# Performance work log

Hardware: AMD Instinct MI355X
Metric: run time of the kernel (lower is better)

## Reference

```python
import jax, jax.numpy as jnp
import numpy as np

N, F_IN, H, MH = 50000, 128, 128, 256
E = 800000

def _lin_init(key, out_d, in_d, bias=True):
    k1, k2 = jax.random.split(key)
    bound = 1.0 / np.sqrt(in_d)
    W = jax.random.uniform(k1, (out_d, in_d), minval=-bound, maxval=bound, dtype=jnp.float32)
    if bias:
        b = jax.random.uniform(k2, (out_d,), minval=-bound, maxval=bound, dtype=jnp.float32)
        return W, b
    return W, None

def setup_inputs() -> dict:
    key = jax.random.key(0)
    ks = jax.random.split(key, 8)
    x = jax.random.normal(ks[0], (N, F_IN), dtype=jnp.float32)
    edge_index = jax.random.randint(ks[1], (2, E), 0, N, dtype=jnp.int64)
    W1l, b1l = _lin_init(ks[2], H, F_IN, bias=True)   # SAGEConv1 neighbor lin (with bias)
    W1r, _ = _lin_init(ks[3], H, F_IN, bias=False)    # SAGEConv1 root lin (no bias)
    W2l, b2l = _lin_init(ks[4], H, H, bias=True)
    W2r, _ = _lin_init(ks[5], H, H, bias=False)
    Wm1, bm1 = _lin_init(ks[6], MH, 2 * H, bias=True)
    Wm2, bm2 = _lin_init(ks[7], 1, MH, bias=True)
    return {"x": x, "edge_index": edge_index,
            "W1l": W1l, "b1l": b1l, "W1r": W1r,
            "W2l": W2l, "b2l": b2l, "W2r": W2r,
            "Wm1": Wm1, "bm1": bm1, "Wm2": Wm2, "bm2": bm2}

def _sage_conv(x, src, dst, Wl, bl, Wr, num_nodes):
    # mean-aggregate messages x[src] at dst, then lin_l(agg) + lin_r(x)
    agg = jax.ops.segment_sum(x[src], dst, num_segments=num_nodes)
    cnt = jax.ops.segment_sum(jnp.ones((src.shape[0],), x.dtype), dst, num_segments=num_nodes)
    agg = agg / jnp.maximum(cnt, 1.0)[:, None]
    return agg @ Wl.T + bl + x @ Wr.T

def reference(x, edge_index, W1l, b1l, W1r, W2l, b2l, W2r, Wm1, bm1, Wm2, bm2):
    src, dst = edge_index[0], edge_index[1]
    n = x.shape[0]
    h = jax.nn.relu(_sage_conv(x, src, dst, W1l, b1l, W1r, n))
    # dropout is identity in eval mode
    h = jax.nn.relu(_sage_conv(h, src, dst, W2l, b2l, W2r, n))
    ef = jnp.concatenate([h[src], h[dst]], axis=-1)  # [E, 2H]
    out = jax.nn.relu(ef @ Wm1.T + bm1) @ Wm2.T + bm2
    return out.reshape(-1)
```

## Files before the change

kernel.cpp:

```cpp
#include <hip/hip_runtime.h>
#include <hip/hip_bf16.h>

#define NN 50000
#define F 128
#define EE 800000
#define MHD 256
#define CAP 44

typedef __attribute__((ext_vector_type(8))) short bf16x8;
typedef __attribute__((ext_vector_type(4))) float f32x4;

__device__ __forceinline__ float b2f(unsigned short u) {
    union { unsigned int i; float f; } v; v.i = ((unsigned)u) << 16; return v.f;
}
__device__ __forceinline__ unsigned short f2b(float f) {
    unsigned int x = __float_as_uint(f);
    unsigned int r = x + 0x7fffu + ((x >> 16) & 1u);
    return (unsigned short)(r >> 16);
}

__global__ __launch_bounds__(256) void cast_zero_kernel(
    const float* __restrict__ x,
    const float* __restrict__ W1l, const float* __restrict__ W1r,
    const float* __restrict__ W2l, const float* __restrict__ W2r,
    const float* __restrict__ Wm1, const float* __restrict__ Wm2,
    unsigned short* __restrict__ xb, unsigned short* __restrict__ wb,
    int* __restrict__ cntp, float* __restrict__ w2p) {
    int bid = blockIdx.x;
    if (bid < 6250) {
        int i = (bid * 256 + threadIdx.x) * 4;
        float4 v = *(const float4*)(x + i);
        ushort4 o; o.x = f2b(v.x); o.y = f2b(v.y); o.z = f2b(v.z); o.w = f2b(v.w);
        *(ushort4*)(xb + i) = o;
    } else if (bid < 6378) {
        int i = ((bid - 6250) * 256 + threadIdx.x) * 4;
        unsigned short o[4];
        if (i < 32768) {
            const float* p = (i < 16384) ? (W1l + i) : (W1r + (i - 16384));
            float4 v = *(const float4*)p;
            o[0] = f2b(v.x); o[1] = f2b(v.y); o[2] = f2b(v.z); o[3] = f2b(v.w);
        } else if (i < 65536) {
            int local = i - 32768;
            const float* M = (local < 16384) ? W2l : W2r;
            int lm = local & 16383;
            int n = lm >> 7, kp = lm & 127;
#pragma unroll
            for (int t = 0; t < 4; t++) {
                int k = ((kp + t) & 7) * 16 + ((kp + t) >> 3);
                o[t] = f2b(M[n * 128 + k]);
            }
        } else {
            int local = i - 65536;
            int n = local >> 8, k2 = local & 255;
            int half = k2 >> 7, kp = k2 & 127;
#pragma unroll
            for (int t = 0; t < 4; t++) {
                int k = half * 128 + ((kp + t) & 7) * 16 + ((kp + t) >> 3);
                o[t] = f2b(Wm1[n * 256 + k]);
            }
        }
        *(ushort4*)(wb + i) = *(ushort4*)o;
    } else if (bid < 7160) {
        int idx = ((bid - 6378) * 256 + threadIdx.x) * 4;
        if (idx < NN * 16) *(int4*)(cntp + idx) = (int4){0, 0, 0, 0};
    } else {
        int t = threadIdx.x;
        w2p[t] = Wm2[(t & 15) * 16 + (t >> 4)];
    }
}

__global__ __launch_bounds__(256) void cvt_fill_kernel(
    const int* __restrict__ ei, int* __restrict__ cntp,
    unsigned short* __restrict__ slots) {
    __shared__ int isI64;
    if (threadIdx.x == 0) {
        int z = 0;
        for (int i = 1; i < 128; i += 2) z |= ei[i];
        isI64 = (z == 0) ? 1 : 0;
    }
    __syncthreads();
    int e = blockIdx.x * 256 + threadIdx.x;
    if (e >= EE) return;
    int s, d;
    if (isI64) {
        const long long* e64 = (const long long*)ei;
        s = (int)e64[e];
        d = (int)e64[EE + e];
    } else {
        s = ei[e];
        d = ei[EE + e];
    }
    int pos = atomicAdd(&cntp[d << 4], 1);
    if (pos < CAP) {
        unsigned short* sp = slots + (size_t)d * (CAP * 3) + pos * 3;
        sp[0] = (unsigned short)s;
        sp[1] = (unsigned short)(e & 0xffff);
        sp[2] = (unsigned short)((unsigned)e >> 16);
    }
}

__global__ __launch_bounds__(256) void sage_layer_kernel(
    const unsigned short* __restrict__ xin,
    const unsigned short* __restrict__ slots, const int* __restrict__ cntp,
    int* __restrict__ cnt2,
    const unsigned short* __restrict__ W1, const unsigned short* __restrict__ W2,
    const float* __restrict__ bias,
    unsigned short* __restrict__ out) {
    __shared__ unsigned short lds[4][16][136];
    int wave = threadIdx.x >> 6, lane = threadIdx.x & 63;
    int m0 = (blockIdx.x * 4 + wave) * 16;

    int g = lane >> 4, l16 = lane & 15, col8 = l16 * 8;
    for (int batch = 0; batch < 4; batch++) {
        int node = m0 + batch * 4 + g;
        int n = 0, ctrue = 0;
        const unsigned short* sp = slots;
        if (node < NN) {
            ctrue = cntp[node << 4];
            n = (ctrue < CAP) ? ctrue : CAP;
            sp = slots + (size_t)node * (CAP * 3);
            if (l16 == 0) cnt2[node] = ctrue;
        }
        float a[8] = {0,0,0,0,0,0,0,0};
        float b[8] = {0,0,0,0,0,0,0,0};
        int j = 0;
        for (; j + 7 < n; j += 8) {
            int s0 = sp[(j + 0) * 3], s1 = sp[(j + 1) * 3];
            int s2 = sp[(j + 2) * 3], s3 = sp[(j + 3) * 3];
            int s4 = sp[(j + 4) * 3], s5 = sp[(j + 5) * 3];
            int s6 = sp[(j + 6) * 3], s7 = sp[(j + 7) * 3];
            bf16x8 v0 = *(const bf16x8*)(xin + (size_t)s0 * F + col8);
            bf16x8 v1 = *(const bf16x8*)(xin + (size_t)s1 * F + col8);
            bf16x8 v2 = *(const bf16x8*)(xin + (size_t)s2 * F + col8);
            bf16x8 v3 = *(const bf16x8*)(xin + (size_t)s3 * F + col8);
            bf16x8 v4 = *(const bf16x8*)(xin + (size_t)s4 * F + col8);
            bf16x8 v5 = *(const bf16x8*)(xin + (size_t)s5 * F + col8);
            bf16x8 v6 = *(const bf16x8*)(xin + (size_t)s6 * F + col8);
            bf16x8 v7 = *(const bf16x8*)(xin + (size_t)s7 * F + col8);
            for (int i = 0; i < 8; i++)
                a[i] += (b2f((unsigned short)v0[i]) + b2f((unsigned short)v1[i]))
                      + (b2f((unsigned short)v2[i]) + b2f((unsigned short)v3[i]));
            for (int i = 0; i < 8; i++)
                b[i] += (b2f((unsigned short)v4[i]) + b2f((unsigned short)v5[i]))
                      + (b2f((unsigned short)v6[i]) + b2f((unsigned short)v7[i]));
        }
        for (; j + 3 < n; j += 4) {
            int s0 = sp[(j + 0) * 3], s1 = sp[(j + 1) * 3];
            int s2 = sp[(j + 2) * 3], s3 = sp[(j + 3) * 3];
            bf16x8 v0 = *(const bf16x8*)(xin + (size_t)s0 * F + col8);
            bf16x8 v1 = *(const bf16x8*)(xin + (size_t)s1 * F + col8);
            bf16x8 v2 = *(const bf16x8*)(xin + (size_t)s2 * F + col8);
            bf16x8 v3 = *(const bf16x8*)(xin + (size_t)s3 * F + col8);
            for (int i = 0; i < 8; i++)
                a[i] += (b2f((unsigned short)v0[i]) + b2f((unsigned short)v1[i]))
                      + (b2f((unsigned short)v2[i]) + b2f((unsigned short)v3[i]));
        }
        for (; j < n; j++) {
            int s0 = sp[j * 3];
            bf16x8 v0 = *(const bf16x8*)(xin + (size_t)s0 * F + col8);
            for (int i = 0; i < 8; i++) a[i] += b2f((unsigned short)v0[i]);
        }
        float inv = 1.0f / fmaxf((float)ctrue, 1.0f);
        unsigned short o[8];
        for (int i = 0; i < 8; i++) o[i] = f2b((a[i] + b[i]) * inv);
        *(bf16x8*)&lds[wave][batch * 4 + g][col8] = *(bf16x8*)o;
    }
    __syncthreads();

    int c = lane & 15, q = lane >> 4;
    f32x4 acc[8];
    for (int nt = 0; nt < 8; nt++) {
        float b = bias[nt * 16 + c];
        acc[nt] = (f32x4){b, b, b, b};
    }
    int mrow = m0 + c; if (mrow > NN - 1) mrow = NN - 1;
    for (int op = 0; op < 2; op++) {
        const unsigned short* W = op ? W2 : W1;
        for (int kb = 0; kb < 4; kb++) {
            bf16x8 a;
            if (op == 0) a = *(const bf16x8*)&lds[wave][c][kb * 32 + q * 8];
            else         a = *(const bf16x8*)(xin + (size_t)mrow * F + kb * 32 + q * 8);
            for (int nt = 0; nt < 8; nt++) {
                bf16x8 b = *(const bf16x8*)(W + (size_t)(nt * 16 + c) * F + kb * 32 + q * 8);
                acc[nt] = __builtin_amdgcn_mfma_f32_16x16x32_bf16(a, b, acc[nt], 0, 0, 0);
            }
        }
    }
#pragma unroll
    for (int r = 0; r < 4; r++) {
        int node = m0 + q * 4 + r;
        if (node < NN) {
            unsigned short o[8];
#pragma unroll
            for (int nt = 0; nt < 8; nt++) o[nt] = f2b(fmaxf(acc[nt][r], 0.0f));
            *(bf16x8*)(out + (size_t)node * F + c * 8) = *(bf16x8*)o;
        }
    }
}

__global__ __launch_bounds__(256) void pq_gemm_kernel(
    const unsigned short* __restrict__ h,
    const unsigned short* __restrict__ wmb,
    const float* __restrict__ bm1,
    unsigned short* __restrict__ PQ) {
    int wave = threadIdx.x >> 6, lane = threadIdx.x & 63;
    int c = lane & 15, q = lane >> 4;
    int half = wave >> 1, ntBase = (wave & 1) * 8;
    int m0 = blockIdx.x * 64;
    int mr0 = m0 + c;      if (mr0 > NN - 1) mr0 = NN - 1;
    int mr1 = m0 + 16 + c; if (mr1 > NN - 1) mr1 = NN - 1;
    int mr2 = m0 + 32 + c; if (mr2 > NN - 1) mr2 = NN - 1;
    int mr3 = m0 + 48 + c; if (mr3 > NN - 1) mr3 = NN - 1;
    f32x4 acc0[8], acc1[8], acc2[8], acc3[8];
#pragma unroll
    for (int nt = 0; nt < 8; nt++) {
        float b = half ? bm1[(ntBase + nt) * 16 + c] : 0.0f;
        acc0[nt] = (f32x4){b, b, b, b};
        acc1[nt] = (f32x4){b, b, b, b};
        acc2[nt] = (f32x4){b, b, b, b};
        acc3[nt] = (f32x4){b, b, b, b};
    }
#pragma unroll
    for (int kb = 0; kb < 4; kb++) {
        bf16x8 a0 = *(const bf16x8*)(h + (size_t)mr0 * F + kb * 32 + q * 8);
        bf16x8 a1 = *(const bf16x8*)(h + (size_t)mr1 * F + kb * 32 + q * 8);
        bf16x8 a2 = *(const bf16x8*)(h + (size_t)mr2 * F + kb * 32 + q * 8);
        bf16x8 a3 = *(const bf16x8*)(h + (size_t)mr3 * F + kb * 32 + q * 8);
#pragma unroll
        for (int nt = 0; nt < 8; nt++) {
            bf16x8 b = *(const bf16x8*)(wmb + (size_t)((ntBase + nt) * 16 + c) * 256 + half * 128 + kb * 32 + q * 8);
            acc0[nt] = __builtin_amdgcn_mfma_f32_16x16x32_bf16(a0, b, acc0[nt], 0, 0, 0);
            acc1[nt] = __builtin_amdgcn_mfma_f32_16x16x32_bf16(a1, b, acc1[nt], 0, 0, 0);
            acc2[nt] = __builtin_amdgcn_mfma_f32_16x16x32_bf16(a2, b, acc2[nt], 0, 0, 0);
            acc3[nt] = __builtin_amdgcn_mfma_f32_16x16x32_bf16(a3, b, acc3[nt], 0, 0, 0);
        }
    }
#pragma unroll
    for (int r = 0; r < 4; r++) {
        int n0 = m0 + q * 4 + r;
        int n1 = m0 + 16 + q * 4 + r;
        int n2 = m0 + 32 + q * 4 + r;
        int n3 = m0 + 48 + q * 4 + r;
        unsigned short o[8];
        if (n0 < NN) {
#pragma unroll
            for (int nt = 0; nt < 8; nt++) o[nt] = f2b(acc0[nt][r]);
            *(bf16x8*)(PQ + (size_t)n0 * 512 + half * 256 + c * 16 + ntBase) = *(bf16x8*)o;
        }
        if (n1 < NN) {
#pragma unroll
            for (int nt = 0; nt < 8; nt++) o[nt] = f2b(acc1[nt][r]);
            *(bf16x8*)(PQ + (size_t)n1 * 512 + half * 256 + c * 16 + ntBase) = *(bf16x8*)o;
        }
        if (n2 < NN) {
#pragma unroll
            for (int nt = 0; nt < 8; nt++) o[nt] = f2b(acc2[nt][r]);
            *(bf16x8*)(PQ + (size_t)n2 * 512 + half * 256 + c * 16 + ntBase) = *(bf16x8*)o;
        }
        if (n3 < NN) {
#pragma unroll
            for (int nt = 0; nt < 8; nt++) o[nt] = f2b(acc3[nt][r]);
            *(bf16x8*)(PQ + (size_t)n3 * 512 + half * 256 + c * 16 + ntBase) = *(bf16x8*)o;
        }
    }
}

__global__ __launch_bounds__(256) void edge_dot_kernel(
    const unsigned short* __restrict__ PQ,
    const unsigned short* __restrict__ slots, const int* __restrict__ cnt2,
    const float* __restrict__ w2p, const float* __restrict__ bm2,
    float* __restrict__ out) {
    int wave = threadIdx.x >> 6, lane = threadIdx.x & 63;
    int node = blockIdx.x * 4 + wave;
    if (node >= NN) return;
    int g = lane >> 4, l16 = lane & 15;
    int col = l16 * 16;
    float w2f[16], qf[16];
    *(float4*)(w2f + 0)  = *(const float4*)(w2p + col + 0);
    *(float4*)(w2f + 4)  = *(const float4*)(w2p + col + 4);
    *(float4*)(w2f + 8)  = *(const float4*)(w2p + col + 8);
    *(float4*)(w2f + 12) = *(const float4*)(w2p + col + 12);
    {
        bf16x8 q0 = *(const bf16x8*)(PQ + (size_t)node * 512 + 256 + col);
        bf16x8 q1 = *(const bf16x8*)(PQ + (size_t)node * 512 + 256 + col + 8);
#pragma unroll
        for (int i = 0; i < 8; i++) { qf[i] = b2f((unsigned short)q0[i]); qf[8 + i] = b2f((unsigned short)q1[i]); }
    }
    float b2 = bm2[0];
    int ctrue = cnt2[node];
    int n = (ctrue < CAP) ? ctrue : CAP;
    const unsigned short* sp = slots + (size_t)node * (CAP * 3);
    int j = g;
    for (; j + 4 < n; j += 8) {
        int s0 = sp[j * 3],       s1 = sp[(j + 4) * 3];
        int eid0 = sp[j * 3 + 1] | ((int)sp[j * 3 + 2] << 16);
        int eid1 = sp[(j + 4) * 3 + 1] | ((int)sp[(j + 4) * 3 + 2] << 16);
        uint4 a0 = *(const uint4*)(PQ + (size_t)s0 * 512 + col);
        uint4 a1 = *(const uint4*)(PQ + (size_t)s0 * 512 + col + 8);
        uint4 c0 = *(const uint4*)(PQ + (size_t)s1 * 512 + col);
        uint4 c1 = *(const uint4*)(PQ + (size_t)s1 * 512 + col + 8);
        float t0 = 0.f, t1 = 0.f;
        unsigned int w0[8] = {a0.x, a0.y, a0.z, a0.w, a1.x, a1.y, a1.z, a1.w};
        unsigned int w1[8] = {c0.x, c0.y, c0.z, c0.w, c1.x, c1.y, c1.z, c1.w};
#pragma unroll
        for (int i = 0; i < 8; i++) {
            float lo0 = __uint_as_float(w0[i] << 16);
            float hi0 = __uint_as_float(w0[i] & 0xffff0000u);
            float lo1 = __uint_as_float(w1[i] << 16);
            float hi1 = __uint_as_float(w1[i] & 0xffff0000u);
            t0 += fmaxf(lo0 + qf[2 * i], 0.f) * w2f[2 * i]
                + fmaxf(hi0 + qf[2 * i + 1], 0.f) * w2f[2 * i + 1];
            t1 += fmaxf(lo1 + qf[2 * i], 0.f) * w2f[2 * i]
                + fmaxf(hi1 + qf[2 * i + 1], 0.f) * w2f[2 * i + 1];
        }
        t0 += __shfl_xor(t0, 1);  t1 += __shfl_xor(t1, 1);
        t0 += __shfl_xor(t0, 2);  t1 += __shfl_xor(t1, 2);
        t0 += __shfl_xor(t0, 4);  t1 += __shfl_xor(t1, 4);
        t0 += __shfl_xor(t0, 8);  t1 += __shfl_xor(t1, 8);
        if (l16 == 0) { out[eid0] = t0 + b2; out[eid1] = t1 + b2; }
    }
    for (; j < n; j += 4) {
        int s0 = sp[j * 3];
        int eid0 = sp[j * 3 + 1] | ((int)sp[j * 3 + 2] << 16);
        uint4 a0 = *(const uint4*)(PQ + (size_t)s0 * 512 + col);
        uint4 a1 = *(const uint4*)(PQ + (size_t)s0 * 512 + col + 8);
        unsigned int w0[8] = {a0.x, a0.y, a0.z, a0.w, a1.x, a1.y, a1.z, a1.w};
        float t = 0.f;
#pragma unroll
        for (int i = 0; i < 8; i++) {
            float lo = __uint_as_float(w0[i] << 16);
            float hi = __uint_as_float(w0[i] & 0xffff0000u);
            t += fmaxf(lo + qf[2 * i], 0.f) * w2f[2 * i]
               + fmaxf(hi + qf[2 * i + 1], 0.f) * w2f[2 * i + 1];
        }
        t += __shfl_xor(t, 1);
        t += __shfl_xor(t, 2);
        t += __shfl_xor(t, 4);
        t += __shfl_xor(t, 8);
        if (l16 == 0) out[eid0] = t + b2;
    }
}

extern "C" void kernel_launch(void* const* d_in, const int* in_sizes, int n_in,
                              void* d_out, int out_size, void* d_ws, size_t ws_size,
                              hipStream_t stream) {
    const float* x   = (const float*)d_in[0];
    const int*   ei  = (const int*)d_in[1];
    const float* W1l = (const float*)d_in[2];
    const float* b1l = (const float*)d_in[3];
    const float* W1r = (const float*)d_in[4];
    const float* W2l = (const float*)d_in[5];
    const float* b2l = (const float*)d_in[6];
    const float* W2r = (const float*)d_in[7];
    const float* Wm1 = (const float*)d_in[8];
    const float* bm1 = (const float*)d_in[9];
    const float* Wm2 = (const float*)d_in[10];
    const float* bm2 = (const float*)d_in[11];

    char* ws = (char*)d_ws;
    unsigned short* PQ    = (unsigned short*)(ws);
    unsigned short* xb    = (unsigned short*)(ws);
    unsigned short* h1    = (unsigned short*)(ws + 12800000);
    int*            cntp  = (int*)(ws + 25600000);
    unsigned short* wb    = (unsigned short*)(ws + 51200000);
    float*          w2p   = (float*)(ws + 51462144);
    int*            cnt2  = (int*)(ws + 51463168);
    unsigned short* slots = (unsigned short*)(ws + 51663168);
    unsigned short* h2    = (unsigned short*)(ws + 64863168);
    float*          outp  = (float*)d_out;

    const unsigned short* w1l_b  = wb;
    const unsigned short* w1r_b  = wb + 16384;
    const unsigned short* w2l_p  = wb + 32768;
    const unsigned short* w2r_p  = wb + 49152;
    const unsigned short* wm1_p  = wb + 65536;

    cast_zero_kernel<<<7161, 256, 0, stream>>>(x, W1l, W1r, W2l, W2r, Wm1, Wm2, xb, wb, cntp, w2p);
    cvt_fill_kernel<<<3125, 256, 0, stream>>>(ei, cntp, slots);

    sage_layer_kernel<<<782, 256, 0, stream>>>(xb, slots, cntp, cnt2, w1l_b, w1r_b, b1l, h1);
    sage_layer_kernel<<<782, 256, 0, stream>>>(h1, slots, cntp, cnt2, w2l_p, w2r_p, b2l, h2);
    pq_gemm_kernel<<<782, 256, 0, stream>>>(h2, wm1_p, bm1, PQ);
    edge_dot_kernel<<<12500, 256, 0, stream>>>(PQ, slots, cnt2, w2p, bm2, outp);
}
```

Baseline: 369.8 us.

## Build CSR slots via two-pass bucketing with LDS staging instead of global atomics

Replaces the per-edge global atomic scatter into padded per-node counters and slots with two passes. First edges are binned into coarse buckets of 64 destination nodes, split 8 ways. Then one block per bucket assembles the slot lists in LDS and writes them out contiguously. This avoids scattered global atomics and the write of a 3.2MB zeroed counter array, at the cost of an extra kernel and an intermediate bucket buffer with capacity limits (BCAP=256 per cell) that could silently drop edges under skewed degree.

Measured after the change: 372.4 us. About the same (+0.7%).

```diff
diff --git a/kernel.cpp b/kernel.cpp
--- a/kernel.cpp
+++ b/kernel.cpp
@@ -6,6 +6,8 @@
 #define EE 800000
 #define MHD 256
 #define CAP 44
+#define NBKT 782
+#define BCAP 256
 
 typedef __attribute__((ext_vector_type(8))) short bf16x8;
 typedef __attribute__((ext_vector_type(4))) float f32x4;
@@ -25,7 +27,7 @@
     const float* __restrict__ W2l, const float* __restrict__ W2r,
     const float* __restrict__ Wm1, const float* __restrict__ Wm2,
     unsigned short* __restrict__ xb, unsigned short* __restrict__ wb,
-    int* __restrict__ cntp, float* __restrict__ w2p) {
+    int* __restrict__ bcnt, float* __restrict__ w2p) {
     int bid = blockIdx.x;
     if (bid < 6250) {
         int i = (bid * 256 + threadIdx.x) * 4;
@@ -60,18 +62,18 @@
             }
         }
         *(ushort4*)(wb + i) = *(ushort4*)o;
-    } else if (bid < 7160) {
+    } else if (bid < 6385) {
         int idx = ((bid - 6378) * 256 + threadIdx.x) * 4;
-        if (idx < NN * 16) *(int4*)(cntp + idx) = (int4){0, 0, 0, 0};
+        if (idx < 8 * NBKT) *(int4*)(bcnt + idx) = (int4){0, 0, 0, 0};
     } else {
         int t = threadIdx.x;
         w2p[t] = Wm2[(t & 15) * 16 + (t >> 4)];
     }
 }
 
-__global__ __launch_bounds__(256) void cvt_fill_kernel(
-    const int* __restrict__ ei, int* __restrict__ cntp,
-    unsigned short* __restrict__ slots) {
+__global__ __launch_bounds__(256) void bucket_kernel(
+    const int* __restrict__ ei, int* __restrict__ bcnt,
+    int2* __restrict__ bkt) {
     __shared__ int isI64;
     if (threadIdx.x == 0) {
         int z = 0;
@@ -90,19 +92,54 @@
         s = ei[e];
         d = ei[EE + e];
     }
-    int pos = atomicAdd(&cntp[d << 4], 1);
-    if (pos < CAP) {
-        unsigned short* sp = slots + (size_t)d * (CAP * 3) + pos * 3;
-        sp[0] = (unsigned short)s;
-        sp[1] = (unsigned short)(e & 0xffff);
-        sp[2] = (unsigned short)((unsigned)e >> 16);
+    int cell = (blockIdx.x & 7) * NBKT + (d >> 6);
+    int pos = atomicAdd(&bcnt[cell], 1);
+    if (pos < BCAP) {
+        bkt[(size_t)cell * BCAP + pos] = make_int2((int)((unsigned)s | ((unsigned)d << 16)), e);
+    }
+}
+
+__global__ __launch_bounds__(256) void build_kernel(
+    const int* __restrict__ bcnt, const int2* __restrict__ bkt,
+    unsigned short* __restrict__ slots, int* __restrict__ cnt2) {
+    __shared__ unsigned short stg[64][132];
+    __shared__ int lcnt[64];
+    int b = blockIdx.x, t = threadIdx.x;
+    if (t < 64) lcnt[t] = 0;
+    __syncthreads();
+#pragma unroll
+    for (int seg = 0; seg < 8; seg++) {
+        int cell = seg * NBKT + b;
+        int bc = bcnt[cell]; if (bc > BCAP) bc = BCAP;
+        for (int i = t; i < bc; i += 256) {
+            int2 en = bkt[(size_t)cell * BCAP + i];
+            unsigned v = (unsigned)en.x;
+            int s = (int)(v & 0xffffu);
+            int dl = (int)((v >> 16) & 63u);
+            int pos = atomicAdd(&lcnt[dl], 1);
+            if (pos < CAP) {
+                stg[dl][pos * 3 + 0] = (unsigned short)s;
+                stg[dl][pos * 3 + 1] = (unsigned short)(en.y & 0xffff);
+                stg[dl][pos * 3 + 2] = (unsigned short)((unsigned)en.y >> 16);
+            }
+        }
+    }
+    __syncthreads();
+    for (int v = t; v < 64 * 33; v += 256) {
+        int row = v / 33, off = (v % 33) * 4;
+        int node = b * 64 + row;
+        if (node < NN)
+            *(ushort4*)(slots + (size_t)node * 132 + off) = *(ushort4*)&stg[row][off];
+    }
+    if (t < 64) {
+        int node = b * 64 + t;
+        if (node < NN) cnt2[node] = lcnt[t];
     }
 }
 
 __global__ __launch_bounds__(256) void sage_layer_kernel(
     const unsigned short* __restrict__ xin,
-    const unsigned short* __restrict__ slots, const int* __restrict__ cntp,
-    int* __restrict__ cnt2,
+    const unsigned short* __restrict__ slots, const int* __restrict__ cnt2,
     const unsigned short* __restrict__ W1, const unsigned short* __restrict__ W2,
     const float* __restrict__ bias,
     unsigned short* __restrict__ out) {
@@ -116,10 +153,9 @@
         int n = 0, ctrue = 0;
         const unsigned short* sp = slots;
         if (node < NN) {
-            ctrue = cntp[node << 4];
+            ctrue = cnt2[node];
             n = (ctrue < CAP) ? ctrue : CAP;
             sp = slots + (size_t)node * (CAP * 3);
-            if (l16 == 0) cnt2[node] = ctrue;
         }
         float a[8] = {0,0,0,0,0,0,0,0};
         float b[8] = {0,0,0,0,0,0,0,0};
@@ -361,12 +397,13 @@
     unsigned short* PQ    = (unsigned short*)(ws);
     unsigned short* xb    = (unsigned short*)(ws);
     unsigned short* h1    = (unsigned short*)(ws + 12800000);
-    int*            cntp  = (int*)(ws + 25600000);
+    int2*           bkt   = (int2*)(ws + 25600000);
     unsigned short* wb    = (unsigned short*)(ws + 51200000);
     float*          w2p   = (float*)(ws + 51462144);
     int*            cnt2  = (int*)(ws + 51463168);
-    unsigned short* slots = (unsigned short*)(ws + 51663168);
-    unsigned short* h2    = (unsigned short*)(ws + 64863168);
+    int*            bcnt  = (int*)(ws + 51663168);
+    unsigned short* slots = (unsigned short*)(ws + 51688256);
+    unsigned short* h2    = (unsigned short*)(ws + 64888256);
     float*          outp  = (float*)d_out;
 
     const unsigned short* w1l_b  = wb;
@@ -375,11 +412,12 @@
     const unsigned short* w2r_p  = wb + 49152;
     const unsigned short* wm1_p  = wb + 65536;
 
-    cast_zero_kernel<<<7161, 256, 0, stream>>>(x, W1l, W1r, W2l, W2r, Wm1, Wm2, xb, wb, cntp, w2p);
-    cvt_fill_kernel<<<3125, 256, 0, stream>>>(ei, cntp, slots);
-
-    sage_layer_kernel<<<782, 256, 0, stream>>>(xb, slots, cntp, cnt2, w1l_b, w1r_b, b1l, h1);
-    sage_layer_kernel<<<782, 256, 0, stream>>>(h1, slots, cntp, cnt2, w2l_p, w2r_p, b2l, h2);
+    cast_zero_kernel<<<6386, 256, 0, stream>>>(x, W1l, W1r, W2l, W2r, Wm1, Wm2, xb, wb, bcnt, w2p);
+    bucket_kernel<<<3125, 256, 0, stream>>>(ei, bcnt, bkt);
+    build_kernel<<<NBKT, 256, 0, stream>>>(bcnt, bkt, slots, cnt2);
+
+    sage_layer_kernel<<<782, 256, 0, stream>>>(xb, slots, cnt2, w1l_b, w1r_b, b1l, h1);
+    sage_layer_kernel<<<782, 256, 0, stream>>>(h1, slots, cnt2, w2l_p, w2r_p, b2l, h2);
     pq_gemm_kernel<<<782, 256, 0, stream>>>(h2, wm1_p, bm1, PQ);
     edge_dot_kernel<<<12500, 256, 0, stream>>>(PQ, slots, cnt2, w2p, bm2, outp);
 }
```

## Fuse edge bucketing with casts, compact degree counters, drop cnt2 copy

Applied to the files above, without the earlier changes.

The edge-bucketing atomics move into the same kernel as the x and weight bf16 casts, so both run in one launch that can overlap atomic-heavy and bandwidth-heavy blocks. A small separate zero kernel clears the counters first. The counter array goes from a 64-byte-padded stride (d<<4) to a dense int array, which cuts zeroing traffic from 3.2MB to 200KB. The extra cnt2 copy written by the sage kernel is removed. Denser counters may increase atomic contention on shared cache lines.

Result: faster. 362.5 us (-2.0%).

```diff
diff --git a/kernel.cpp b/kernel.cpp
--- a/kernel.cpp
+++ b/kernel.cpp
@@ -19,21 +19,60 @@
     return (unsigned short)(r >> 16);
 }
 
-__global__ __launch_bounds__(256) void cast_zero_kernel(
+__global__ __launch_bounds__(256) void zero_kernel(
+    int* __restrict__ cnt, const float* __restrict__ Wm2, float* __restrict__ w2p) {
+    int bid = blockIdx.x;
+    if (bid < 49) {
+        int idx = (bid * 256 + threadIdx.x) * 4;
+        if (idx < NN) *(int4*)(cnt + idx) = (int4){0, 0, 0, 0};
+    } else {
+        int t = threadIdx.x;
+        w2p[t] = Wm2[(t & 15) * 16 + (t >> 4)];
+    }
+}
+
+__global__ __launch_bounds__(256) void prep_kernel(
+    const int* __restrict__ ei, int* __restrict__ cnt,
+    unsigned short* __restrict__ slots,
     const float* __restrict__ x,
     const float* __restrict__ W1l, const float* __restrict__ W1r,
     const float* __restrict__ W2l, const float* __restrict__ W2r,
-    const float* __restrict__ Wm1, const float* __restrict__ Wm2,
-    unsigned short* __restrict__ xb, unsigned short* __restrict__ wb,
-    int* __restrict__ cntp, float* __restrict__ w2p) {
+    const float* __restrict__ Wm1,
+    unsigned short* __restrict__ xb, unsigned short* __restrict__ wb) {
     int bid = blockIdx.x;
-    if (bid < 6250) {
-        int i = (bid * 256 + threadIdx.x) * 4;
+    if (bid < 3125) {
+        __shared__ int isI64;
+        if (threadIdx.x == 0) {
+            int z = 0;
+            for (int i = 1; i < 128; i += 2) z |= ei[i];
+            isI64 = (z == 0) ? 1 : 0;
+        }
+        __syncthreads();
+        int e = bid * 256 + threadIdx.x;
+        if (e >= EE) return;
+        int s, d;
+        if (isI64) {
+            const long long* e64 = (const long long*)ei;
+            s = (int)e64[e];
+            d = (int)e64[EE + e];
+        } else {
+            s = ei[e];
+            d = ei[EE + e];
+        }
+        int pos = atomicAdd(&cnt[d], 1);
+        if (pos < CAP) {
+            unsigned short* sp = slots + (size_t)d * (CAP * 3) + pos * 3;
+            sp[0] = (unsigned short)s;
+            sp[1] = (unsigned short)(e & 0xffff);
+            sp[2] = (unsigned short)((unsigned)e >> 16);
+        }
+    } else if (bid < 9375) {
+        int i = ((bid - 3125) * 256 + threadIdx.x) * 4;
         float4 v = *(const float4*)(x + i);
         ushort4 o; o.x = f2b(v.x); o.y = f2b(v.y); o.z = f2b(v.z); o.w = f2b(v.w);
         *(ushort4*)(xb + i) = o;
-    } else if (bid < 6378) {
-        int i = ((bid - 6250) * 256 + threadIdx.x) * 4;
+    } else {
+        int i = ((bid - 9375) * 256 + threadIdx.x) * 4;
         unsigned short o[4];
         if (i < 32768) {
             const float* p = (i < 16384) ? (W1l + i) : (W1r + (i - 16384));
@@ -60,49 +99,12 @@
             }
         }
         *(ushort4*)(wb + i) = *(ushort4*)o;
-    } else if (bid < 7160) {
-        int idx = ((bid - 6378) * 256 + threadIdx.x) * 4;
-        if (idx < NN * 16) *(int4*)(cntp + idx) = (int4){0, 0, 0, 0};
-    } else {
-        int t = threadIdx.x;
-        w2p[t] = Wm2[(t & 15) * 16 + (t >> 4)];
-    }
-}
-
-__global__ __launch_bounds__(256) void cvt_fill_kernel(
-    const int* __restrict__ ei, int* __restrict__ cntp,
-    unsigned short* __restrict__ slots) {
-    __shared__ int isI64;
-    if (threadIdx.x == 0) {
-        int z = 0;
-        for (int i = 1; i < 128; i += 2) z |= ei[i];
-        isI64 = (z == 0) ? 1 : 0;
-    }
-    __syncthreads();
-    int e = blockIdx.x * 256 + threadIdx.x;
-    if (e >= EE) return;
-    int s, d;
-    if (isI64) {
-        const long long* e64 = (const long long*)ei;
-        s = (int)e64[e];
-        d = (int)e64[EE + e];
-    } else {
-        s = ei[e];
-        d = ei[EE + e];
-    }
-    int pos = atomicAdd(&cntp[d << 4], 1);
-    if (pos < CAP) {
-        unsigned short* sp = slots + (size_t)d * (CAP * 3) + pos * 3;
-        sp[0] = (unsigned short)s;
-        sp[1] = (unsigned short)(e & 0xffff);
-        sp[2] = (unsigned short)((unsigned)e >> 16);
     }
 }
 
 __global__ __launch_bounds__(256) void sage_layer_kernel(
     const unsigned short* __restrict__ xin,
-    const unsigned short* __restrict__ slots, const int* __restrict__ cntp,
-    int* __restrict__ cnt2,
+    const unsigned short* __restrict__ slots, const int* __restrict__ cnt,
     const unsigned short* __restrict__ W1, const unsigned short* __restrict__ W2,
     const float* __restrict__ bias,
     unsigned short* __restrict__ out) {
@@ -116,10 +118,9 @@
         int n = 0, ctrue = 0;
         const unsigned short* sp = slots;
         if (node < NN) {
-            ctrue = cntp[node << 4];
+            ctrue = cnt[node];
             n = (ctrue < CAP) ? ctrue : CAP;
             sp = slots + (size_t)node * (CAP * 3);
-            if (l16 == 0) cnt2[node] = ctrue;
         }
         float a[8] = {0,0,0,0,0,0,0,0};
         float b[8] = {0,0,0,0,0,0,0,0};
@@ -267,7 +268,7 @@
 
 __global__ __launch_bounds__(256) void edge_dot_kernel(
     const unsigned short* __restrict__ PQ,
-    const unsigned short* __restrict__ slots, const int* __restrict__ cnt2,
+    const unsigned short* __restrict__ slots, const int* __restrict__ cnt,
     const float* __restrict__ w2p, const float* __restrict__ bm2,
     float* __restrict__ out) {
     int wave = threadIdx.x >> 6, lane = threadIdx.x & 63;
@@ -287,7 +288,7 @@
         for (int i = 0; i < 8; i++) { qf[i] = b2f((unsigned short)q0[i]); qf[8 + i] = b2f((unsigned short)q1[i]); }
     }
     float b2 = bm2[0];
-    int ctrue = cnt2[node];
+    int ctrue = cnt[node];
     int n = (ctrue < CAP) ? ctrue : CAP;
     const unsigned short* sp = slots + (size_t)node * (CAP * 3);
     int j = g;
@@ -361,10 +362,9 @@
     unsigned short* PQ    = (unsigned short*)(ws);
     unsigned short* xb    = (unsigned short*)(ws);
     unsigned short* h1    = (unsigned short*)(ws + 12800000);
-    int*            cntp  = (int*)(ws + 25600000);
     unsigned short* wb    = (unsigned short*)(ws + 51200000);
     float*          w2p   = (float*)(ws + 51462144);
-    int*            cnt2  = (int*)(ws + 51463168);
+    int*            cnt   = (int*)(ws + 51463168);
     unsigned short* slots = (unsigned short*)(ws + 51663168);
     unsigned short* h2    = (unsigned short*)(ws + 64863168);
     float*          outp  = (float*)d_out;
@@ -375,11 +375,11 @@
     const unsigned short* w2r_p  = wb + 49152;
     const unsigned short* wm1_p  = wb + 65536;
 
-    cast_zero_kernel<<<7161, 256, 0, stream>>>(x, W1l, W1r, W2l, W2r, Wm1, Wm2, xb, wb, cntp, w2p);
-    cvt_fill_kernel<<<3125, 256, 0, stream>>>(ei, cntp, slots);
-
-    sage_layer_kernel<<<782, 256, 0, stream>>>(xb, slots, cntp, cnt2, w1l_b, w1r_b, b1l, h1);
-    sage_layer_kernel<<<782, 256, 0, stream>>>(h1, slots, cntp, cnt2, w2l_p, w2r_p, b2l, h2);
+    zero_kernel<<<50, 256, 0, stream>>>(cnt, Wm2, w2p);
+    prep_kernel<<<9503, 256, 0, stream>>>(ei, cnt, slots, x, W1l, W1r, W2l, W2r, Wm1, xb, wb);
+
+    sage_layer_kernel<<<782, 256, 0, stream>>>(xb, slots, cnt, w1l_b, w1r_b, b1l, h1);
+    sage_layer_kernel<<<782, 256, 0, stream>>>(h1, slots, cnt, w2l_p, w2r_p, b2l, h2);
     pq_gemm_kernel<<<782, 256, 0, stream>>>(h2, wm1_p, bm1, PQ);
-    edge_dot_kernel<<<12500, 256, 0, stream>>>(PQ, slots, cnt2, w2p, bm2, outp);
-}
+    edge_dot_kernel<<<12500, 256, 0, stream>>>(PQ, slots, cnt, w2p, bm2, outp);
+}
```
